# Kernel tuning notes

Measured on AMD Instinct MI355X. Metric: run time of the kernel, lower is better.

The kernel has to match this reference:

```python
import jax, jax.numpy as jnp
import numpy as np

D_MODEL = 2048
N_HEADS = 32
N_KV = 8
HEAD_DIM = D_MODEL // N_HEADS  # 64
D_FF = 8192
ROPE_BASE = 10000.0
EPS = 1e-5
B, S = 2, 2048


def setup_inputs() -> dict:
    key = jax.random.key(0)
    ks = jax.random.split(key, 8)
    s = 0.02
    qkv_out = (N_HEADS + 2 * N_KV) * HEAD_DIM
    return {
        "x": jax.random.normal(ks[0], (B, S, D_MODEL), jnp.float32),
        "w_norm1": jnp.ones((D_MODEL,), jnp.float32),
        "w_qkv": jax.random.normal(ks[1], (D_MODEL, qkv_out), jnp.float32) * s,
        "w_out": jax.random.normal(ks[2], (D_MODEL, D_MODEL), jnp.float32) * s,
        "w_norm2": jnp.ones((D_MODEL,), jnp.float32),
        "w_gate": jax.random.normal(ks[3], (D_MODEL, D_FF), jnp.float32) * s,
        "w_up": jax.random.normal(ks[4], (D_MODEL, D_FF), jnp.float32) * s,
        "w_down": jax.random.normal(ks[5], (D_FF, D_MODEL), jnp.float32) * s,
    }


def _rmsnorm(x, w):
    var = jnp.mean(x * x, axis=-1, keepdims=True)
    return x * jax.lax.rsqrt(var + EPS) * w


def _rope(x, cos, sin):
    # x: [b, s, h, d]; cos/sin: [s, d/2]; non-interleaved (NeoX half split)
    half = x.shape[-1] // 2
    x1, x2 = x[..., :half], x[..., half:]
    c = cos[None, :, None, :]
    sn = sin[None, :, None, :]
    return jnp.concatenate([x1 * c - x2 * sn, x1 * sn + x2 * c], axis=-1)


def _forward(x, w_norm1, w_qkv, w_out, w_norm2, w_gate, w_up, w_down):
    b, s, d = x.shape
    # --- attention block ---
    h = _rmsnorm(x, w_norm1)
    qkv = h @ w_qkv  # [b, s, (H + 2*KV) * hd]
    q = qkv[..., : N_HEADS * HEAD_DIM].reshape(b, s, N_HEADS, HEAD_DIM)
    kv = qkv[..., N_HEADS * HEAD_DIM:].reshape(b, s, 2, N_KV, HEAD_DIM)
    k, v = kv[:, :, 0], kv[:, :, 1]

    inv_freq = 1.0 / (ROPE_BASE ** (jnp.arange(0, HEAD_DIM, 2, dtype=jnp.float32) / HEAD_DIM))
    t = jnp.arange(s, dtype=jnp.float32)
    freqs = t[:, None] * inv_freq[None, :]  # [s, hd/2]
    cos, sin = jnp.cos(freqs), jnp.sin(freqs)
    q = _rope(q, cos, sin)
    k = _rope(k, cos, sin)

    # GQA: repeat_interleave kv heads to match q heads
    g = N_HEADS // N_KV
    k = jnp.repeat(k, g, axis=2)  # [b, s, H, hd]
    v = jnp.repeat(v, g, axis=2)

    scale = 1.0 / np.sqrt(HEAD_DIM)
    scores = jnp.einsum("bqhd,bkhd->bhqk", q, k) * scale
    causal = jnp.tril(jnp.ones((s, s), bool))
    scores = jnp.where(causal[None, None], scores, jnp.finfo(scores.dtype).min)
    attn = jax.nn.softmax(scores, axis=-1)
    ctx = jnp.einsum("bhqk,bkhd->bqhd", attn, v).reshape(b, s, N_HEADS * HEAD_DIM)
    x = x + ctx @ w_out

    # --- MLP block (SwiGLU) ---
    h2 = _rmsnorm(x, w_norm2)
    mlp = (jax.nn.silu(h2 @ w_gate) * (h2 @ w_up)) @ w_down
    return x + mlp


def reference(x, w_norm1, w_qkv, w_out, w_norm2, w_gate, w_up, w_down):
    return _forward(x, w_norm1, w_qkv, w_out, w_norm2, w_gate, w_up, w_down)
```

## Files before the change

kernel.cpp:

```cpp
#include <hip/hip_runtime.h>
#include <stdint.h>

#define D_MODEL 2048
#define S_LEN   2048
#define NTOK    4096
#define QKV_N   3072
#define DFF     8192

typedef float  f32x4   __attribute__((ext_vector_type(4)));
typedef float  f32x16  __attribute__((ext_vector_type(16)));
typedef __bf16 bf16x8  __attribute__((ext_vector_type(8)));
typedef unsigned short u16;
typedef unsigned short u16x8 __attribute__((ext_vector_type(8)));

__device__ __forceinline__ float b2f(u16 u){ union{float f; uint32_t i;} v; v.i = ((uint32_t)u) << 16; return v.f; }
__device__ __forceinline__ u16 f2b(float f){
  union{float f; uint32_t i;} v; v.f = f;
  uint32_t r = v.i + 0x7FFFu + ((v.i >> 16) & 1u);
  return (u16)(r >> 16);
}

__device__ __forceinline__ void gload_lds16(const void* gsrc, void* ldst){
  __builtin_amdgcn_global_load_lds(
      (const __attribute__((address_space(1))) void*)gsrc,
      (__attribute__((address_space(3))) void*)ldst,
      16, 0, 0);
}

__device__ __forceinline__ void conv_tiles(const float* W, const float* W2, u16* WT,
    int Nfull, int Kt, int Nt, int k0g, int n0g, int rmul, void* ldsbuf)
{
  if (W == nullptr) return;
  float* tf = (float*)ldsbuf;
  const int tt  = threadIdx.x;
  const int nTn = Nt >> 6;
  const int nT  = (Kt >> 6) * nTn;
  const int bid = (blockIdx.z * gridDim.y + blockIdx.y) * gridDim.x + blockIdx.x;
  const int gsz = gridDim.x * gridDim.y * gridDim.z;
  const int c4 = (tt & 15) << 2;
  const int r  = tt >> 4;
  for (int tile = bid; tile < nT; tile += gsz) {
    const int k0 = (tile / nTn) << 6, n0 = (tile % nTn) << 6;
    for (int m = 0; m < 2; ++m) {
      const float* Ws = m ? W2 : W;
      if (m && W2 == nullptr) break;
      __syncthreads();
      if (tt < 256) {
#pragma unroll
        for (int i = 0; i < 4; ++i) {
          int row = r + i * 16;
          float4 v = *reinterpret_cast<const float4*>(&Ws[(size_t)(k0g + k0 + row) * Nfull + n0g + n0 + c4]);
          tf[row * 65 + c4 + 0] = v.x; tf[row * 65 + c4 + 1] = v.y;
          tf[row * 65 + c4 + 2] = v.z; tf[row * 65 + c4 + 3] = v.w;
        }
      }
      __syncthreads();
      if (tt < 256) {
#pragma unroll
        for (int i = 0; i < 4; ++i) {
          int n = r + i * 16;
          ushort4 ov;
          ov.x = f2b(tf[(c4 + 0) * 65 + n]); ov.y = f2b(tf[(c4 + 1) * 65 + n]);
          ov.z = f2b(tf[(c4 + 2) * 65 + n]); ov.w = f2b(tf[(c4 + 3) * 65 + n]);
          *reinterpret_cast<ushort4*>(&WT[(size_t)((n0 + n) * rmul + m) * Kt + k0 + c4]) = ov;
        }
      }
    }
  }
}

__global__ void sincos_kernel(float* __restrict__ ct, float* __restrict__ st)
{
  int idx = blockIdx.x * 256 + threadIdx.x;
  if (idx >= S_LEN * 32) return;
  int p = idx >> 5, i = idx & 31;
  double freq = pow(10000.0, -((double)(2*i)) / 64.0);
  double ang  = (double)p * freq;
  ct[idx] = (float)cos(ang);
  st[idx] = (float)sin(ang);
}

template<bool BF16IN>
__global__ __launch_bounds__(256) void rmsnorm_kernel(const void* __restrict__ xin, const float* __restrict__ w, u16* __restrict__ out,
                                                      const float* cvW, const float* cvW2, u16* cvWT, int cvNfull, int cvKt, int cvNt, int cvK0g, int cvN0g, int cvRm)
{
  __shared__ float tfbuf[64 * 65];
  const int row = blockIdx.x;
  const int t = threadIdx.x;
  float v[8];
  if (BF16IN) {
    const u16* xr = ((const u16*)xin) + (size_t)row * D_MODEL;
    u16x8 a = *reinterpret_cast<const u16x8*>(&xr[t*8]);
#pragma unroll
    for (int j = 0; j < 8; ++j) v[j] = b2f(a[j]);
  } else {
    const float* xr = ((const float*)xin) + (size_t)row * D_MODEL;
    float4 a = *reinterpret_cast<const float4*>(&xr[t*8]);
    float4 c = *reinterpret_cast<const float4*>(&xr[t*8+4]);
    v[0]=a.x; v[1]=a.y; v[2]=a.z; v[3]=a.w; v[4]=c.x; v[5]=c.y; v[6]=c.z; v[7]=c.w;
  }
  float ss = 0.f;
#pragma unroll
  for (int j = 0; j < 8; ++j) ss += v[j]*v[j];
#pragma unroll
  for (int d = 1; d < 64; d <<= 1) ss += __shfl_xor(ss, d);
  __shared__ float red[4];
  if ((t & 63) == 0) red[t >> 6] = ss;
  __syncthreads();
  ss = red[0] + red[1] + red[2] + red[3];
  const float sc = rsqrtf(ss * (1.0f / (float)D_MODEL) + 1e-5f);
  float4 w0 = *reinterpret_cast<const float4*>(&w[t*8]);
  float4 w1 = *reinterpret_cast<const float4*>(&w[t*8+4]);
  u16x8 o;
  o[0]=f2b(v[0]*sc*w0.x); o[1]=f2b(v[1]*sc*w0.y); o[2]=f2b(v[2]*sc*w0.z); o[3]=f2b(v[3]*sc*w0.w);
  o[4]=f2b(v[4]*sc*w1.x); o[5]=f2b(v[5]*sc*w1.y); o[6]=f2b(v[6]*sc*w1.z); o[7]=f2b(v[7]*sc*w1.w);
  *reinterpret_cast<u16x8*>(&out[(size_t)row * D_MODEL + t*8]) = o;
  conv_tiles(cvW, cvW2, cvWT, cvNfull, cvKt, cvNt, cvK0g, cvN0g, cvRm, tfbuf);
}

template<int EPI>
__device__ __forceinline__ void epi_store(size_t idx, float v, float* Cf, u16* Cb,
                                          const float* resf, const u16* resb, const u16* other)
{
  if (EPI == 2)      Cb[idx] = f2b(v / (1.0f + __expf(-v)));
  else if (EPI == 3) Cb[idx] = f2b(v * b2f(other[idx]));
  else if (EPI == 4) Cb[idx] = f2b(v);
  else if (EPI == 5) Cf[idx] += v;
  else if (EPI == 6) Cb[idx] = f2b(v + resf[idx]);
  else if (EPI == 7) Cf[idx] = v + b2f(resb[idx]);
  else if (EPI == 9) {
    float pv = __shfl_xor(v, 1);
    float gate = (threadIdx.x & 1) ? pv : v;
    float up   = (threadIdx.x & 1) ? v  : pv;
    if (!(threadIdx.x & 1)) Cb[idx] = f2b(gate / (1.0f + __expf(-gate)) * up);
  }
}

template<int EPI>
__global__ __launch_bounds__(512, 2) void gemm8p_kernel(
    const u16* __restrict__ A, const u16* __restrict__ BT, const u16* __restrict__ BT2,
    int K, int lda, int ldb, int ldc, int n_off,
    float* Cf, u16* Cb,
    const float* __restrict__ resf, const u16* __restrict__ resb, const u16* other,
    const float* cvW, const float* cvW2, u16* cvWT, int cvNfull, int cvKt, int cvNt, int cvK0g, int cvN0g, int cvRm)
{
  __shared__ u16 lds[65536];
  const int tid = threadIdx.x;
  const int w = tid >> 6, lane = tid & 63;
  const int g = lane >> 4, lr = lane & 15;
  const int wm = w >> 2, wn = w & 3;
  int fid = blockIdx.y * gridDim.x + blockIdx.x;
  const int nwg = gridDim.x * gridDim.y;
  fid = (fid & 7) * (nwg >> 3) + (fid >> 3);
  const int bn = fid / gridDim.y, bm = fid % gridDim.y;
  const int NT = K >> 6;
  const int NI = NT >> 1;

  const int srow = tid >> 3;
  const int sg   = (tid & 7) ^ (srow & 7);
  const u16* Asrc = A + (size_t)(bm * 256) * lda;
  const u16* Bsrc;
  if (EPI == 9) Bsrc = (bn < 16) ? BT + (size_t)(bn * 256) * ldb
                                 : BT2 + (size_t)(bn * 256 - 4096) * ldb;
  else          Bsrc = BT + (size_t)(bn * 256) * ldb;

  const int agc0 = ((0 + g) ^ (lr & 7)) * 8;
  const int agc1 = ((4 + g) ^ (lr & 7)) * 8;

  f32x4 acc[8][4];
#pragma unroll
  for (int i = 0; i < 8; ++i)
#pragma unroll
    for (int j = 0; j < 4; ++j) acc[i][j] = (f32x4){0.f, 0.f, 0.f, 0.f};
  bf16x8 af[4][2], bf0[2][2], bf1[2][2];

#define STAGE_H(isB, h, b, T) do {                                           \
    int tc = ((T) < NT) ? (T) : (NT - 1);                                    \
    const u16* sb = (isB) ? Bsrc : Asrc;                                     \
    const int  sld = (isB) ? ldb : lda;                                      \
    const u16* s0 = sb + (size_t)((h)*128 + srow) * sld + tc*64 + sg*8;      \
    u16* dst = &lds[(b)*32768 + (isB)*16384 + (h)*8192 + tid*8];             \
    gload_lds16(s0, dst);                                                    \
    gload_lds16(s0 + (size_t)64 * sld, dst + 4096);                          \
  } while (0)

#define LOADA(mih, b) { _Pragma("unroll") for (int q = 0; q < 4; ++q) {      \
    const u16* rp = &lds[(b)*32768 + (wm*128 + (mih)*64 + q*16 + lr) * 64];  \
    af[q][0] = *(const bf16x8*)(rp + agc0);                                  \
    af[q][1] = *(const bf16x8*)(rp + agc1); } }

#define LOADB(dst, nih, b) { _Pragma("unroll") for (int nq = 0; nq < 2; ++nq) { \
    const u16* rp = &lds[(b)*32768 + 16384 + (wn*64 + (nih)*32 + nq*16 + lr) * 64]; \
    dst[nq][0] = *(const bf16x8*)(rp + agc0);                                \
    dst[nq][1] = *(const bf16x8*)(rp + agc1); } }

#define MM(mih, nih, BF) {                                                   \
    __builtin_amdgcn_s_setprio(1);                                           \
    _Pragma("unroll") for (int kk = 0; kk < 2; ++kk)                         \
      _Pragma("unroll") for (int q = 0; q < 4; ++q)                          \
        _Pragma("unroll") for (int nq = 0; nq < 2; ++nq)                     \
          acc[(mih)*4+q][(nih)*2+nq] = __builtin_amdgcn_mfma_f32_16x16x32_bf16( \
              af[q][kk], BF[nq][kk], acc[(mih)*4+q][(nih)*2+nq], 0, 0, 0);   \
    __builtin_amdgcn_s_setprio(0); }

#define PHEND     __builtin_amdgcn_s_barrier();
#define PHEND_VM  asm volatile("s_waitcnt vmcnt(4)" ::: "memory");           \
                  __builtin_amdgcn_s_barrier();

  STAGE_H(0, 0, 0, 0); STAGE_H(0, 1, 0, 0);
  STAGE_H(1, 0, 0, 0); STAGE_H(1, 1, 0, 0);
  STAGE_H(1, 0, 1, 1); STAGE_H(1, 1, 1, 1);
  asm volatile("s_waitcnt vmcnt(4)" ::: "memory");
  __builtin_amdgcn_s_barrier();

  for (int i = 0; i < NI; ++i) {
    const int t0 = 2 * i;
    LOADA(0, 0); LOADB(bf0, 0, 0);
    STAGE_H(0, 0, 1, t0 + 1);
    MM(0, 0, bf0); PHEND;
    LOADB(bf1, 1, 0);
    STAGE_H(0, 1, 1, t0 + 1);
    MM(0, 1, bf1); PHEND;
    LOADA(1, 0);
    STAGE_H(1, 0, 0, t0 + 2);
    MM(1, 1, bf1); PHEND;
    STAGE_H(1, 1, 0, t0 + 2);
    MM(1, 0, bf0); PHEND_VM;
    LOADA(0, 1); LOADB(bf0, 0, 1);
    STAGE_H(0, 0, 0, t0 + 2);
    MM(0, 0, bf0); PHEND;
    LOADB(bf1, 1, 1);
    STAGE_H(0, 1, 0, t0 + 2);
    MM(0, 1, bf1); PHEND;
    LOADA(1, 1);
    STAGE_H(1, 0, 1, t0 + 3);
    MM(1, 1, bf1); PHEND;
    STAGE_H(1, 1, 1, t0 + 3);
    MM(1, 0, bf0); PHEND_VM;
  }
#undef STAGE_H
#undef LOADA
#undef LOADB
#undef MM

#pragma unroll
  for (int mi = 0; mi < 8; ++mi) {
    const int rowOff = (mi >> 2) * 64 + (mi & 3) * 16;
#pragma unroll
    for (int ni = 0; ni < 4; ++ni) {
      const int colOff = (ni >> 1) * 32 + (ni & 1) * 16;
#pragma unroll
      for (int j = 0; j < 4; ++j) {
        int row = bm*256 + wm*128 + rowOff + g*4 + j;
        int col = n_off + bn*256 + wn*64 + colOff + lr;
        size_t idx = (EPI == 9) ? ((size_t)row * ldc + (col >> 1))
                                : ((size_t)row * ldc + col);
        epi_store<EPI>(idx, acc[mi][ni][j], Cf, Cb, resf, resb, other);
      }
    }
  }
  conv_tiles(cvW, cvW2, cvWT, cvNfull, cvKt, cvNt, cvK0g, cvN0g, cvRm, lds);
}

template<int EPI>
__global__ __launch_bounds__(512) void gemm128_kernel(
    const u16* __restrict__ A, const u16* __restrict__ BT,
    int K, int lda, int ldb, int ldc, int n_off,
    float* Cf, u16* Cb,
    const float* __restrict__ resf, const u16* __restrict__ resb, const u16* other,
    const float* c1W, const float* c1W2, u16* c1WT, int c1Nfull, int c1Kt, int c1Nt, int c1K0g, int c1N0g, int c1Rm,
    const float* c2W, const float* c2W2, u16* c2WT, int c2Nfull, int c2Kt, int c2Nt, int c2K0g, int c2N0g, int c2Rm)
{
  __shared__ u16 lds[49152];
  const int tid = threadIdx.x;
  const int w = tid >> 6, lane = tid & 63;
  const int g = lane >> 4, lr = lane & 15;
  const int wm = w >> 2, wn = w & 3;
  int fid = blockIdx.y * gridDim.x + blockIdx.x;
  const int nwg = gridDim.x * gridDim.y;
  fid = (fid & 7) * (nwg >> 3) + (fid >> 3);
  const int bn = fid / gridDim.y, bm = fid % gridDim.y;
  const int NT = K >> 6;
  const int NI = NT >> 1;

  const int srow = tid >> 3;
  const int sg   = (tid & 7) ^ (srow & 7);
  const u16* Asrc = A  + (size_t)(bm * 128) * lda;
  const u16* Bsrc = BT + (size_t)(bn * 256) * ldb;

  const int agc0 = ((0 + g) ^ (lr & 7)) * 8;
  const int agc1 = ((4 + g) ^ (lr & 7)) * 8;

  f32x4 acc[4][4];
#pragma unroll
  for (int i = 0; i < 4; ++i)
#pragma unroll
    for (int j = 0; j < 4; ++j) acc[i][j] = (f32x4){0.f, 0.f, 0.f, 0.f};
  bf16x8 af[2][2], bf0[2][2], bf1[2][2];

#define STAGE_A(b, T) do {                                                   \
    int tc = ((T) < NT) ? (T) : (NT - 1);                                    \
    const u16* s0 = Asrc + (size_t)srow * lda + tc*64 + sg*8;                \
    u16* dst = &lds[(b)*24576 + tid*8];                                      \
    gload_lds16(s0, dst);                                                    \
    gload_lds16(s0 + (size_t)64 * lda, dst + 4096);                          \
  } while (0)

#define STAGE_BH(h, b, T) do {                                               \
    int tc = ((T) < NT) ? (T) : (NT - 1);                                    \
    const u16* s0 = Bsrc + (size_t)((h)*128 + srow) * ldb + tc*64 + sg*8;    \
    u16* dst = &lds[(b)*24576 + 8192 + (h)*8192 + tid*8];                    \
    gload_lds16(s0, dst);                                                    \
    gload_lds16(s0 + (size_t)64 * ldb, dst + 4096);                         \
  } while (0)

#define LOADA(mih, b) { _Pragma("unroll") for (int q = 0; q < 2; ++q) {      \
    const u16* rp = &lds[(b)*24576 + (wm*64 + (mih)*32 + q*16 + lr) * 64];   \
    af[q][0] = *(const bf16x8*)(rp + agc0);                                  \
    af[q][1] = *(const bf16x8*)(rp + agc1); } }

#define LOADB(dst, nih, b) { _Pragma("unroll") for (int nq = 0; nq < 2; ++nq) { \
    const u16* rp = &lds[(b)*24576 + 8192 + (wn*64 + (nih)*32 + nq*16 + lr) * 64]; \
    dst[nq][0] = *(const bf16x8*)(rp + agc0);                                \
    dst[nq][1] = *(const bf16x8*)(rp + agc1); } }

#define MM(mih, nih, BF) {                                                   \
    __builtin_amdgcn_s_setprio(1);                                           \
    _Pragma("unroll") for (int kk = 0; kk < 2; ++kk)                         \
      _Pragma("unroll") for (int q = 0; q < 2; ++q)                          \
        _Pragma("unroll") for (int nq = 0; nq < 2; ++nq)                     \
          acc[(mih)*2+q][(nih)*2+nq] = __builtin_amdgcn_mfma_f32_16x16x32_bf16( \
              af[q][kk], BF[nq][kk], acc[(mih)*2+q][(nih)*2+nq], 0, 0, 0);   \
    __builtin_amdgcn_s_setprio(0); }

#define PHEND     __builtin_amdgcn_s_barrier();

  STAGE_A(0, 0); STAGE_BH(0, 0, 0); STAGE_BH(1, 0, 0);
  STAGE_BH(0, 1, 1); STAGE_BH(1, 1, 1);
  asm volatile("s_waitcnt vmcnt(4)" ::: "memory");
  __builtin_amdgcn_s_barrier();

  for (int i = 0; i < NI; ++i) {
    const int t0 = 2 * i;
    LOADA(0, 0); LOADB(bf0, 0, 0);
    STAGE_A(1, t0 + 1);
    MM(0, 0, bf0); PHEND;
    LOADB(bf1, 1, 0);
    STAGE_BH(0, 0, t0 + 2);
    MM(0, 1, bf1); PHEND;
    LOADA(1, 0);
    STAGE_BH(1, 0, t0 + 2);
    MM(1, 1, bf1); PHEND;
    STAGE_A(0, t0 + 2);
    MM(1, 0, bf0);
    asm volatile("s_waitcnt vmcnt(6)" ::: "memory");
    __builtin_amdgcn_s_barrier();
    LOADA(0, 1); LOADB(bf0, 0, 1);
    MM(0, 0, bf0); PHEND;
    LOADB(bf1, 1, 1);
    STAGE_BH(0, 1, t0 + 3);
    MM(0, 1, bf1); PHEND;
    LOADA(1, 1);
    STAGE_BH(1, 1, t0 + 3);
    MM(1, 1, bf1); PHEND;
    MM(1, 0, bf0);
    asm volatile("s_waitcnt vmcnt(4)" ::: "memory");
    __builtin_amdgcn_s_barrier();
  }
#undef STAGE_A
#undef STAGE_BH
#undef LOADA
#undef LOADB
#undef MM
#undef PHEND

#pragma unroll
  for (int mi = 0; mi < 4; ++mi) {
    const int rowOff = (mi >> 1) * 32 + (mi & 1) * 16;
#pragma unroll
    for (int ni = 0; ni < 4; ++ni) {
      const int colOff = (ni >> 1) * 32 + (ni & 1) * 16;
#pragma unroll
      for (int j = 0; j < 4; ++j) {
        int row = bm*128 + wm*64 + rowOff + g*4 + j;
        int col = n_off + bn*256 + wn*64 + colOff + lr;
        epi_store<EPI>((size_t)row * ldc + col, acc[mi][ni][j], Cf, Cb, resf, resb, other);
      }
    }
  }
  conv_tiles(c1W, c1W2, c1WT, c1Nfull, c1Kt, c1Nt, c1K0g, c1N0g, c1Rm, lds);
  conv_tiles(c2W, c2W2, c2WT, c2Nfull, c2Kt, c2Nt, c2K0g, c2N0g, c2Rm, lds);
}

__global__ __launch_bounds__(256) void rope_kernel(
    const u16* __restrict__ qkv, const float* __restrict__ ct, const float* __restrict__ st,
    u16* __restrict__ Kt, u16* __restrict__ VT)
{
  const int tok = blockIdx.x;
  const int b = tok >> 11, s = tok & (S_LEN - 1);
  const int w = threadIdx.x >> 6, lane = threadIdx.x & 63;
  const size_t base = (size_t)tok * QKV_N;
  for (int slot = w; slot < 16; slot += 4) {
    int col = (slot < 8) ? 2048 + slot * 64 : 2560 + (slot - 8) * 64;
    float v = b2f(qkv[base + col + lane]);
    if (slot < 8) {
      int i = lane & 31;
      float c = ct[s * 32 + i], sn = st[s * 32 + i];
      float p = b2f(qkv[base + col + (lane ^ 32)]);
      v = (lane < 32) ? (v * c - p * sn) : (v * c + p * sn);
    }
    u16 ob = f2b(v);
    if (slot < 8) Kt[((size_t)(b * 8 + slot)     * S_LEN + s) * 64 + lane] = ob;
    else          VT[((size_t)(b * 8 + slot - 8) * 64 + lane) * S_LEN + s] = ob;
  }
}

#define ASCALE 0.1803368801111204f
#define MFIX   16.0f
__global__ __launch_bounds__(256, 2) void attn_kernel(
    const u16* __restrict__ qkv, const u16* __restrict__ Kt,
    const u16* __restrict__ VT, u16* __restrict__ ctx,
    const float* __restrict__ ct, const float* __restrict__ st,
    const float* cvW, const float* cvW2, u16* cvWT, int cvNfull, int cvKt, int cvNt, int cvK0g, int cvN0g, int cvRm)
{
  __shared__ float tfbuf[64 * 65];
  const int fid = blockIdx.y * gridDim.x + blockIdx.x;
  const int idx = fid >> 3;
  const int bh  = (fid & 7) * 8 + (idx & 7);
  const int y   = idx >> 3;
  const int wid = threadIdx.x >> 6;
  const int lane = threadIdx.x & 63;
  const int b = bh >> 5, h = bh & 31;
  const int kvh = (b << 3) + (h >> 2);
  const int jj = y * 4 + wid;
  const int cq = lane & 31;
  const int hi = lane >> 5;

  const int q0a = jj << 5,        nta = jj + 1;
  const int q0b = (63 - jj) << 5, ntb = 64 - jj;

  const u16* Kp = Kt + (size_t)kvh * S_LEN * 64 + cq * 64 + hi * 8;
  const u16* Vbase = VT + (size_t)kvh * 64 * S_LEN + hi * 8;
  const u16* Vp[4];
#pragma unroll
  for (int v = 0; v < 4; ++v)
    Vp[v] = Vbase + (size_t)((v & 1) * 32 + cq) * S_LEN + (v >> 1) * 16;

  __shared__ float xch[4][32];

#define ATT_LOADK(KF, T) { _Pragma("unroll") for (int q_ = 0; q_ < 4; ++q_) \
    KF[q_] = *(const bf16x8*)(Kp + (T) * 2048 + q_ * 16); }
#define ATT_LOADV(VF, T) { _Pragma("unroll") for (int v_ = 0; v_ < 4; ++v_) \
    VF[v_] = *(const bf16x8*)(Vp[v_] + (T) * 32); }

#define ATT_QK(S, KF, QF) do {                                               \
    S = (f32x16){};                                                          \
    S = __builtin_amdgcn_mfma_f32_32x32x16_bf16(KF[0], QF[0], S, 0, 0, 0);   \
    S = __builtin_amdgcn_mfma_f32_32x32x16_bf16(KF[1], QF[1], S, 0, 0, 0);   \
    S = __builtin_amdgcn_mfma_f32_32x32x16_bf16(KF[2], QF[2], S, 0, 0, 0);   \
    S = __builtin_amdgcn_mfma_f32_32x32x16_bf16(KF[3], QF[3], S, 0, 0, 0);   \
  } while (0)

#define ATT_PACK(P, PA0, PA1) do {                                           \
    uint32_t wds[8], pw[8];                                                  \
    _Pragma("unroll") for (int j = 0; j < 8; ++j) {                          \
      uint32_t wv;                                                           \
      asm("v_cvt_pk_bf16_f32 %0, %1, %2" : "=v"(wv) : "v"((P)[2*j]), "v"((P)[2*j+1])); \
      wds[j] = wv;                                                           \
    }                                                                        \
    _Pragma("unroll") for (int j = 0; j < 8; ++j) pw[j] = __shfl_xor(wds[j], 32); \
    PA0.u[0] = hi ? pw[2]  : wds[0];                                         \
    PA0.u[1] = hi ? pw[3]  : wds[1];                                         \
    PA0.u[2] = hi ? wds[2] : pw[0];                                          \
    PA0.u[3] = hi ? wds[3] : pw[1];                                          \
    PA1.u[0] = hi ? pw[6]  : wds[4];                                         \
    PA1.u[1] = hi ? pw[7]  : wds[5];                                         \
    PA1.u[2] = hi ? wds[6] : pw[4];                                          \
    PA1.u[3] = hi ? pw[7] ^ 0 : pw[5];                                       \
  } while (0)

#undef ATT_PACK
#define ATT_PACK(P, PA0, PA1) do {                                           \
    uint32_t wds[8], pw[8];                                                  \
    _Pragma("unroll") for (int j = 0; j < 8; ++j) {                          \
      uint32_t wv;                                                           \
      asm("v_cvt_pk_bf16_f32 %0, %1, %2" : "=v"(wv) : "v"((P)[2*j]), "v"((P)[2*j+1])); \
      wds[j] = wv;                                                           \
    }                                                                        \
    _Pragma("unroll") for (int j = 0; j < 8; ++j) pw[j] = __shfl_xor(wds[j], 32); \
    PA0.u[0] = hi ? pw[2]  : wds[0];                                         \
    PA0.u[1] = hi ? pw[3]  : wds[1];                                         \
    PA0.u[2] = hi ? wds[2] : pw[0];                                          \
    PA0.u[3] = hi ? wds[3] : pw[1];                                          \
    PA1.u[0] = hi ? pw[6]  : wds[4];                                         \
    PA1.u[1] = hi ? pw[7]  : wds[5];                                         \
    PA1.u[2] = hi ? wds[6] : pw[4];                                          \
    PA1.u[3] = hi ? wds[7] : pw[5];                                          \
  } while (0)

#define ATT_FIN(S, VF, O0, O1, L, MASK) do {                                 \
    float p[16];                                                             \
    _Pragma("unroll") for (int r = 0; r < 16; ++r) p[r] = S[r];              \
    if (MASK) {                                                              \
      _Pragma("unroll") for (int r = 0; r < 16; ++r) {                       \
        int kk = (r & 3) + 8 * (r >> 2) + 4 * hi;                            \
        if (kk > cq) p[r] = -1e30f;                                          \
      }                                                                      \
    }                                                                        \
    float ts_ = 0.f;                                                         \
    _Pragma("unroll") for (int r = 0; r < 16; ++r) { p[r] = exp2f(p[r] - MFIX); ts_ += p[r]; } \
    L += ts_;                                                                \
    union { uint32_t u[4]; bf16x8 v; } pa0, pa1;                             \
    ATT_PACK(p, pa0, pa1);                                                   \
    O0 = __builtin_amdgcn_mfma_f32_32x32x16_bf16(pa0.v, VF[0], O0, 0, 0, 0); \
    O0 = __builtin_amdgcn_mfma_f32_32x32x16_bf16(pa1.v, VF[2], O0, 0, 0, 0); \
    O1 = __builtin_amdgcn_mfma_f32_32x32x16_bf16(pa0.v, VF[1], O1, 0, 0, 0); \
    O1 = __builtin_amdgcn_mfma_f32_32x32x16_bf16(pa1.v, VF[3], O1, 0, 0, 0); \
  } while (0)

#define ATT_LOADQ(QF, Q0) do {                                               \
    const u16* Qr = qkv + (size_t)(b * S_LEN + (Q0) + cq) * QKV_N + h * 64 + hi * 8; \
    u16 qr[4][8];                                                            \
    _Pragma("unroll") for (int t = 0; t < 4; ++t)                            \
      *reinterpret_cast<u16x8*>(qr[t]) = *reinterpret_cast<const u16x8*>(Qr + t * 16); \
    const float* cb = ct + (size_t)((Q0) + cq) * 32 + hi * 8;                \
    const float* sb = st + (size_t)((Q0) + cq) * 32 + hi * 8;                \
    union { u16 u[8]; bf16x8 v; } qo[4];                                     \
    _Pragma("unroll") for (int t = 0; t < 2; ++t) {                          \
      float4 c0 = *reinterpret_cast<const float4*>(cb + 16 * t);             \
      float4 c1 = *reinterpret_cast<const float4*>(cb + 16 * t + 4);         \
      float4 s0 = *reinterpret_cast<const float4*>(sb + 16 * t);             \
      float4 s1 = *reinterpret_cast<const float4*>(sb + 16 * t + 4);         \
      float cc[8] = {c0.x,c0.y,c0.z,c0.w, c1.x,c1.y,c1.z,c1.w};              \
      float ssn[8] = {s0.x,s0.y,s0.z,s0.w, s1.x,s1.y,s1.z,s1.w};             \
      _Pragma("unroll") for (int i = 0; i < 8; ++i) {                        \
        float lo = b2f(qr[t][i]), hif = b2f(qr[t + 2][i]);                   \
        qo[t].u[i]     = f2b((lo * cc[i] - hif * ssn[i]) * ASCALE);          \
        qo[t + 2].u[i] = f2b((hif * cc[i] + lo * ssn[i]) * ASCALE);          \
      }                                                                      \
    }                                                                        \
    _Pragma("unroll") for (int t = 0; t < 4; ++t) QF[t] = qo[t].v;           \
  } while (0)

#define ATT_EPI(O0, O1, L, Q0) do {                                          \
    float lv = (L) + __shfl_xor((L), 32);                                    \
    float linv = 1.0f / lv;                                                  \
    if (hi == 0) xch[wid][cq] = linv;                                        \
    asm volatile("s_waitcnt lgkmcnt(0)" ::: "memory");                       \
    __builtin_amdgcn_sched_barrier(0);                                       \
    float4 n0 = *reinterpret_cast<const float4*>(&xch[wid][4 * hi + 0]);     \
    float4 n1 = *reinterpret_cast<const float4*>(&xch[wid][4 * hi + 8]);     \
    float4 n2 = *reinterpret_cast<const float4*>(&xch[wid][4 * hi + 16]);    \
    float4 n3 = *reinterpret_cast<const float4*>(&xch[wid][4 * hi + 24]);    \
    float na[16] = {n0.x,n0.y,n0.z,n0.w, n1.x,n1.y,n1.z,n1.w,                \
                    n2.x,n2.y,n2.z,n2.w, n3.x,n3.y,n3.z,n3.w};               \
    _Pragma("unroll") for (int r = 0; r < 16; ++r) {                         \
      int row = (r & 3) + 8 * (r >> 2) + 4 * hi;                             \
      size_t base_ = (size_t)(b * S_LEN + (Q0) + row) * D_MODEL + h * 64;    \
      ctx[base_ + cq]      = f2b(O0[r] * na[r]);                             \
      ctx[base_ + 32 + cq] = f2b(O1[r] * na[r]);                             \
    }                                                                        \
  } while (0)

#define ATT_STEP(KF, VF, T) do {                                             \
    const bool doA = ((T) < nta);                                            \
    f32x16 sA, sB;                                                           \
    if (doA) ATT_QK(sA, KF, qfA);                                            \
    ATT_QK(sB, KF, qfB);                                                     \
    if (doA) ATT_FIN(sA, VF, oA0, oA1, lA, ((T) == nta - 1));                \
    ATT_FIN(sB, VF, oB0, oB1, lB, ((T) == ntb - 1));                         \
  } while (0)

  bf16x8 qfA[4], qfB[4];
  ATT_LOADQ(qfA, q0a);
  ATT_LOADQ(qfB, q0b);

  f32x16 oA0 = {}, oA1 = {}, oB0 = {}, oB1 = {};
  float lA = 0.f, lB = 0.f;

  bf16x8 kf0[4], vf0[4], kf1[4], vf1[4];
  ATT_LOADK(kf0, 0); ATT_LOADV(vf0, 0);

#pragma unroll 1
  for (int t = 0; t < ntb; ) {
    if (t + 1 < ntb) { ATT_LOADK(kf1, t + 1); ATT_LOADV(vf1, t + 1); }
    ATT_STEP(kf0, vf0, t);
    ++t; if (t >= ntb) break;
    if (t + 1 < ntb) { ATT_LOADK(kf0, t + 1); ATT_LOADV(vf0, t + 1); }
    ATT_STEP(kf1, vf1, t);
    ++t;
  }

  ATT_EPI(oA0, oA1, lA, q0a);
  ATT_EPI(oB0, oB1, lB, q0b);

#undef ATT_LOADK
#undef ATT_LOADV
#undef ATT_QK
#undef ATT_PACK
#undef ATT_FIN
#undef ATT_LOADQ
#undef ATT_EPI
#undef ATT_STEP

  conv_tiles(cvW, cvW2, cvWT, cvNfull, cvKt, cvNt, cvK0g, cvN0g, cvRm, tfbuf);
}

#define NOCV nullptr, nullptr, nullptr, 0, 0, 0, 0, 0, 1
extern "C" void kernel_launch(void* const* d_in, const int* in_sizes, int n_in,
                              void* d_out, int out_size, void* d_ws, size_t ws_size,
                              hipStream_t stream)
{
  const float* x     = (const float*)d_in[0];
  const float* wn1   = (const float*)d_in[1];
  const float* wqkv  = (const float*)d_in[2];
  const float* wout  = (const float*)d_in[3];
  const float* wn2   = (const float*)d_in[4];
  const float* wgate = (const float*)d_in[5];
  const float* wup   = (const float*)d_in[6];
  const float* wdown = (const float*)d_in[7];
  float* out = (float*)d_out;
  char* ws = (char*)d_ws;

  float* cosT = (float*)(ws + 0);
  float* sinT = (float*)(ws + 262144);
  u16*   U1   = (u16*)  (ws + 524288);
  u16*   U2   = (u16*)  (ws + 17301504);
  u16*   x1b  = (u16*)  (ws + 34078720);
  char*  S    = ws + 50855936;
  u16*   hB   = (u16*)(S + 0);
  u16*   qkvB = (u16*)(S + 16777216);
  u16*   kB   = (u16*)(S + 41943040);
  u16*   vtB  = (u16*)(S + 46137344);
  u16*   ctxB = (u16*)(S + 0);
  u16*   h2B  = (u16*)(S + 0);
  u16*   slab = (u16*)(S + 16777216);
  u16*   U7   = (u16*)(S + 50331648);

  sincos_kernel<<<dim3(256), 256, 0, stream>>>(cosT, sinT);
  rmsnorm_kernel<false><<<dim3(NTOK), 256, 0, stream>>>(x, wn1, hB,
      wqkv, nullptr, U1, 3072, 2048, 3072, 0, 0, 1);

  gemm128_kernel<4><<<dim3(12, 32), 512, 0, stream>>>(hB, U1, 2048, 2048, 2048, 3072, 0,
      nullptr, qkvB, nullptr, nullptr, nullptr,
      wout, nullptr, U7, 2048, 2048, 2048, 0, 0, 1, NOCV);
  rope_kernel<<<dim3(NTOK), 256, 0, stream>>>(qkvB, cosT, sinT, kB, vtB);
  attn_kernel<<<dim3(64, 8), 256, 0, stream>>>(qkvB, kB, vtB, ctxB, cosT, sinT,
      wgate, wup, U1, 8192, 2048, 2048, 0, 0, 2);

  gemm128_kernel<6><<<dim3(8, 32), 512, 0, stream>>>(ctxB, U7, 2048, 2048, 2048, 2048, 0,
      nullptr, x1b, x, nullptr, nullptr,
      wgate, wup, U2, 8192, 2048, 2048, 0, 2048, 2, NOCV);

  rmsnorm_kernel<true><<<dim3(NTOK), 256, 0, stream>>>(x1b, wn2, h2B,
      wdown, nullptr, U7, 2048, 4096, 2048, 0, 0, 1);

  gemm8p_kernel<9><<<dim3(32, 16), 512, 0, stream>>>(h2B, U1, U2, 2048, 2048, 2048, 4096, 0,
      nullptr, slab, nullptr, nullptr, nullptr, NOCV);
  gemm128_kernel<7><<<dim3(8, 32), 512, 0, stream>>>(slab, U7, 4096, 4096, 4096, 2048, 0,
      out, nullptr, nullptr, x1b, nullptr,
      wgate, wup, U1, 8192, 2048, 2048, 0, 4096, 2,
      wgate, wup, U2, 8192, 2048, 2048, 0, 6144, 2);
  gemm8p_kernel<9><<<dim3(32, 16), 512, 0, stream>>>(h2B, U1, U2, 2048, 2048, 2048, 4096, 0,
      nullptr, slab, nullptr, nullptr, nullptr,
      wdown, nullptr, U7, 2048, 4096, 2048, 4096, 0, 1);
  gemm128_kernel<5><<<dim3(8, 32), 512, 0, stream>>>(slab, U7, 4096, 4096, 4096, 2048, 0,
      out, nullptr, nullptr, nullptr, nullptr, NOCV, NOCV);
}
```

Baseline: 747.5 us.

## Interleave warp tile ownership and reorder GEMM LDS staging to free buffers earlier

```diff
diff --git a/kernel.cpp b/kernel.cpp
--- a/kernel.cpp
+++ b/kernel.cpp
@@ -185,12 +185,12 @@
   } while (0)
 
 #define LOADA(mih, b) { _Pragma("unroll") for (int q = 0; q < 4; ++q) {      \
-    const u16* rp = &lds[(b)*32768 + (wm*128 + (mih)*64 + q*16 + lr) * 64];  \
+    const u16* rp = &lds[(b)*32768 + ((mih)*128 + wm*64 + q*16 + lr) * 64];  \
     af[q][0] = *(const bf16x8*)(rp + agc0);                                  \
     af[q][1] = *(const bf16x8*)(rp + agc1); } }
 
 #define LOADB(dst, nih, b) { _Pragma("unroll") for (int nq = 0; nq < 2; ++nq) { \
-    const u16* rp = &lds[(b)*32768 + 16384 + (wn*64 + (nih)*32 + nq*16 + lr) * 64]; \
+    const u16* rp = &lds[(b)*32768 + 16384 + ((nih)*128 + wn*32 + nq*16 + lr) * 64]; \
     dst[nq][0] = *(const bf16x8*)(rp + agc0);                                \
     dst[nq][1] = *(const bf16x8*)(rp + agc1); } }
 
@@ -204,55 +204,54 @@
     __builtin_amdgcn_s_setprio(0); }
 
 #define PHEND     __builtin_amdgcn_s_barrier();
-#define PHEND_VM  asm volatile("s_waitcnt vmcnt(4)" ::: "memory");           \
+#define PHEND_VM  asm volatile("s_waitcnt vmcnt(8)" ::: "memory");           \
                   __builtin_amdgcn_s_barrier();
 
-  STAGE_H(0, 0, 0, 0); STAGE_H(0, 1, 0, 0);
-  STAGE_H(1, 0, 0, 0); STAGE_H(1, 1, 0, 0);
-  STAGE_H(1, 0, 1, 1); STAGE_H(1, 1, 1, 1);
-  asm volatile("s_waitcnt vmcnt(4)" ::: "memory");
+  STAGE_H(0, 0, 0, 0); STAGE_H(1, 0, 0, 0); STAGE_H(1, 1, 0, 0); STAGE_H(0, 1, 0, 0);
+  STAGE_H(0, 0, 1, 1); STAGE_H(1, 0, 1, 1); STAGE_H(1, 1, 1, 1); STAGE_H(0, 1, 1, 1);
+  asm volatile("s_waitcnt vmcnt(8)" ::: "memory");
   __builtin_amdgcn_s_barrier();
 
   for (int i = 0; i < NI; ++i) {
     const int t0 = 2 * i;
     LOADA(0, 0); LOADB(bf0, 0, 0);
-    STAGE_H(0, 0, 1, t0 + 1);
     MM(0, 0, bf0); PHEND;
     LOADB(bf1, 1, 0);
-    STAGE_H(0, 1, 1, t0 + 1);
+    STAGE_H(0, 0, 0, t0 + 2); STAGE_H(1, 0, 0, t0 + 2);
     MM(0, 1, bf1); PHEND;
     LOADA(1, 0);
-    STAGE_H(1, 0, 0, t0 + 2);
+    STAGE_H(1, 1, 0, t0 + 2);
     MM(1, 1, bf1); PHEND;
-    STAGE_H(1, 1, 0, t0 + 2);
+    STAGE_H(0, 1, 0, t0 + 2);
     MM(1, 0, bf0); PHEND_VM;
     LOADA(0, 1); LOADB(bf0, 0, 1);
-    STAGE_H(0, 0, 0, t0 + 2);
     MM(0, 0, bf0); PHEND;
     LOADB(bf1, 1, 1);
-    STAGE_H(0, 1, 0, t0 + 2);
+    STAGE_H(0, 0, 1, t0 + 3); STAGE_H(1, 0, 1, t0 + 3);
     MM(0, 1, bf1); PHEND;
     LOADA(1, 1);
-    STAGE_H(1, 0, 1, t0 + 3);
+    STAGE_H(1, 1, 1, t0 + 3);
     MM(1, 1, bf1); PHEND;
-    STAGE_H(1, 1, 1, t0 + 3);
+    STAGE_H(0, 1, 1, t0 + 3);
     MM(1, 0, bf0); PHEND_VM;
   }
 #undef STAGE_H
 #undef LOADA
 #undef LOADB
 #undef MM
+#undef PHEND
+#undef PHEND_VM
 
 #pragma unroll
   for (int mi = 0; mi < 8; ++mi) {
-    const int rowOff = (mi >> 2) * 64 + (mi & 3) * 16;
+    const int rowOff = (mi >> 2) * 128 + wm * 64 + (mi & 3) * 16;
 #pragma unroll
     for (int ni = 0; ni < 4; ++ni) {
-      const int colOff = (ni >> 1) * 32 + (ni & 1) * 16;
+      const int colOff = (ni >> 1) * 128 + wn * 32 + (ni & 1) * 16;
 #pragma unroll
       for (int j = 0; j < 4; ++j) {
-        int row = bm*256 + wm*128 + rowOff + g*4 + j;
-        int col = n_off + bn*256 + wn*64 + colOff + lr;
+        int row = bm*256 + rowOff + g*4 + j;
+        int col = n_off + bn*256 + colOff + lr;
         size_t idx = (EPI == 9) ? ((size_t)row * ldc + (col >> 1))
                                 : ((size_t)row * ldc + col);
         epi_store<EPI>(idx, acc[mi][ni][j], Cf, Cb, resf, resb, other);
@@ -298,12 +297,16 @@
     for (int j = 0; j < 4; ++j) acc[i][j] = (f32x4){0.f, 0.f, 0.f, 0.f};
   bf16x8 af[2][2], bf0[2][2], bf1[2][2];
 
-#define STAGE_A(b, T) do {                                                   \
+#define STAGE_A0(b, T) do {                                                  \
     int tc = ((T) < NT) ? (T) : (NT - 1);                                    \
-    const u16* s0 = Asrc + (size_t)srow * lda + tc*64 + sg*8;                \
-    u16* dst = &lds[(b)*24576 + tid*8];                                      \
-    gload_lds16(s0, dst);                                                    \
-    gload_lds16(s0 + (size_t)64 * lda, dst + 4096);                          \
+    gload_lds16(Asrc + (size_t)srow * lda + tc*64 + sg*8,                    \
+                &lds[(b)*24576 + tid*8]);                                    \
+  } while (0)
+
+#define STAGE_A1(b, T) do {                                                  \
+    int tc = ((T) < NT) ? (T) : (NT - 1);                                    \
+    gload_lds16(Asrc + (size_t)(64 + srow) * lda + tc*64 + sg*8,             \
+                &lds[(b)*24576 + 4096 + tid*8]);                             \
   } while (0)
 
 #define STAGE_BH(h, b, T) do {                                               \
@@ -315,12 +318,12 @@
   } while (0)
 
 #define LOADA(mih, b) { _Pragma("unroll") for (int q = 0; q < 2; ++q) {      \
-    const u16* rp = &lds[(b)*24576 + (wm*64 + (mih)*32 + q*16 + lr) * 64];   \
+    const u16* rp = &lds[(b)*24576 + ((mih)*64 + wm*32 + q*16 + lr) * 64];   \
     af[q][0] = *(const bf16x8*)(rp + agc0);                                  \
     af[q][1] = *(const bf16x8*)(rp + agc1); } }
 
 #define LOADB(dst, nih, b) { _Pragma("unroll") for (int nq = 0; nq < 2; ++nq) { \
-    const u16* rp = &lds[(b)*24576 + 8192 + (wn*64 + (nih)*32 + nq*16 + lr) * 64]; \
+    const u16* rp = &lds[(b)*24576 + 8192 + ((nih)*128 + wn*32 + nq*16 + lr) * 64]; \
     dst[nq][0] = *(const bf16x8*)(rp + agc0);                                \
     dst[nq][1] = *(const bf16x8*)(rp + agc1); } }
 
@@ -334,56 +337,56 @@
     __builtin_amdgcn_s_setprio(0); }
 
 #define PHEND     __builtin_amdgcn_s_barrier();
-
-  STAGE_A(0, 0); STAGE_BH(0, 0, 0); STAGE_BH(1, 0, 0);
-  STAGE_BH(0, 1, 1); STAGE_BH(1, 1, 1);
-  asm volatile("s_waitcnt vmcnt(4)" ::: "memory");
+#define PHEND_VM  asm volatile("s_waitcnt vmcnt(6)" ::: "memory");           \
+                  __builtin_amdgcn_s_barrier();
+
+  STAGE_A0(0, 0); STAGE_BH(0, 0, 0); STAGE_BH(1, 0, 0); STAGE_A1(0, 0);
+  STAGE_A0(1, 1); STAGE_BH(0, 1, 1); STAGE_BH(1, 1, 1); STAGE_A1(1, 1);
+  asm volatile("s_waitcnt vmcnt(6)" ::: "memory");
   __builtin_amdgcn_s_barrier();
 
   for (int i = 0; i < NI; ++i) {
     const int t0 = 2 * i;
     LOADA(0, 0); LOADB(bf0, 0, 0);
-    STAGE_A(1, t0 + 1);
     MM(0, 0, bf0); PHEND;
     LOADB(bf1, 1, 0);
-    STAGE_BH(0, 0, t0 + 2);
+    STAGE_A0(0, t0 + 2); STAGE_BH(0, 0, t0 + 2);
     MM(0, 1, bf1); PHEND;
     LOADA(1, 0);
     STAGE_BH(1, 0, t0 + 2);
     MM(1, 1, bf1); PHEND;
-    STAGE_A(0, t0 + 2);
-    MM(1, 0, bf0);
-    asm volatile("s_waitcnt vmcnt(6)" ::: "memory");
-    __builtin_amdgcn_s_barrier();
+    STAGE_A1(0, t0 + 2);
+    MM(1, 0, bf0); PHEND_VM;
     LOADA(0, 1); LOADB(bf0, 0, 1);
     MM(0, 0, bf0); PHEND;
     LOADB(bf1, 1, 1);
-    STAGE_BH(0, 1, t0 + 3);
+    STAGE_A0(1, t0 + 3); STAGE_BH(0, 1, t0 + 3);
     MM(0, 1, bf1); PHEND;
     LOADA(1, 1);
     STAGE_BH(1, 1, t0 + 3);
     MM(1, 1, bf1); PHEND;
-    MM(1, 0, bf0);
-    asm volatile("s_waitcnt vmcnt(4)" ::: "memory");
-    __builtin_amdgcn_s_barrier();
-  }
-#undef STAGE_A
+    STAGE_A1(1, t0 + 3);
+    MM(1, 0, bf0); PHEND_VM;
+  }
+#undef STAGE_A0
+#undef STAGE_A1
 #undef STAGE_BH
 #undef LOADA
 #undef LOADB
 #undef MM
 #undef PHEND
+#undef PHEND_VM
 
 #pragma unroll
   for (int mi = 0; mi < 4; ++mi) {
-    const int rowOff = (mi >> 1) * 32 + (mi & 1) * 16;
+    const int rowOff = (mi >> 1) * 64 + wm * 32 + (mi & 1) * 16;
 #pragma unroll
     for (int ni = 0; ni < 4; ++ni) {
-      const int colOff = (ni >> 1) * 32 + (ni & 1) * 16;
+      const int colOff = (ni >> 1) * 128 + wn * 32 + (ni & 1) * 16;
 #pragma unroll
       for (int j = 0; j < 4; ++j) {
-        int row = bm*128 + wm*64 + rowOff + g*4 + j;
-        int col = n_off + bn*256 + wn*64 + colOff + lr;
+        int row = bm*128 + rowOff + g*4 + j;
+        int col = n_off + bn*256 + colOff + lr;
         epi_store<EPI>((size_t)row * ldc + col, acc[mi][ni][j], Cf, Cb, resf, resb, other);
       }
     }
@@ -461,25 +464,6 @@
     S = __builtin_amdgcn_mfma_f32_32x32x16_bf16(KF[3], QF[3], S, 0, 0, 0);   \
   } while (0)
 
-#define ATT_PACK(P, PA0, PA1) do {                                           \
-    uint32_t wds[8], pw[8];                                                  \
-    _Pragma("unroll") for (int j = 0; j < 8; ++j) {                          \
-      uint32_t wv;                                                           \
-      asm("v_cvt_pk_bf16_f32 %0, %1, %2" : "=v"(wv) : "v"((P)[2*j]), "v"((P)[2*j+1])); \
-      wds[j] = wv;                                                           \
-    }                                                                        \
-    _Pragma("unroll") for (int j = 0; j < 8; ++j) pw[j] = __shfl_xor(wds[j], 32); \
-    PA0.u[0] = hi ? pw[2]  : wds[0];                                         \
-    PA0.u[1] = hi ? pw[3]  : wds[1];                                         \
-    PA0.u[2] = hi ? wds[2] : pw[0];                                          \
-    PA0.u[3] = hi ? wds[3] : pw[1];                                          \
-    PA1.u[0] = hi ? pw[6]  : wds[4];                                         \
-    PA1.u[1] = hi ? pw[7]  : wds[5];                                         \
-    PA1.u[2] = hi ? wds[6] : pw[4];                                          \
-    PA1.u[3] = hi ? pw[7] ^ 0 : pw[5];                                       \
-  } while (0)
-
-#undef ATT_PACK
 #define ATT_PACK(P, PA0, PA1) do {                                           \
     uint32_t wds[8], pw[8];                                                  \
     _Pragma("unroll") for (int j = 0; j < 8; ++j) {                          \
```

New measurement: 735.4 us. No clear change (-1.6%).
